# Kernel tuning notes

Hardware: AMD Instinct MI355X
Metric: run time of the kernel (lower is better)

The kernel has to match this reference:

```python
import jax, jax.numpy as jnp
import numpy as np

LEAKY_SLOPE = 0.01  # torch nn.LeakyReLU / F.leaky_relu default


def gcn_diffusion(adj, order, feat):
    # A_gcn = adj + I; sym-normalized diffusion D^-1/2 A D^-1/2 applied repeatedly
    B, N, _ = adj.shape
    A = adj + jnp.eye(N, dtype=adj.dtype)
    dinv_sqrt = jnp.sum(A, axis=2) ** -0.5  # [B, N]
    outs = []
    h = feat
    for _ in range(order):
        h = jnp.matmul(A, dinv_sqrt[..., None] * h) * dinv_sqrt[..., None]
        outs.append(h)
    return outs


def scattering_s4(adj, feat):
    # lazy random walk P = 1/2 (I + A D^-1); wavelets Psi_j = P^{2^{j-1}} - P^{2^j}
    dinv = 1.0 / jnp.sum(adj, axis=2)  # [B, N]
    p = feat
    us = []
    for _ in range(8):  # powers P^1 .. P^8
        p = 0.5 * p + 0.5 * jnp.matmul(adj, dinv[..., None] * p)
        us.append(p)
    h1 = feat - us[0]      # I - P
    h2 = us[0] - us[1]     # P - P^2
    h3 = us[1] - us[3]     # P^2 - P^4
    h4 = us[3] - us[7]     # P^4 - P^8
    return h1, h2, h3, h4


def sctconv(X, adj, W1, b1, W2, b2, a, moment):
    leaky = lambda x: jax.nn.leaky_relu(x, LEAKY_SLOPE)
    h = X  # [B, N, F]
    hA, hA2, hA3 = gcn_diffusion(adj, 3, X)
    hA, hA2, hA3 = leaky(hA), leaky(hA2), leaky(hA3)
    s1, s2, s3, s4 = scattering_s4(adj, X)
    mom = jnp.asarray(moment, dtype=X.dtype)
    s1 = jnp.abs(s1) ** mom
    s2 = jnp.abs(s2) ** mom
    s3 = jnp.abs(s3) ** mom
    s4 = jnp.abs(s4) ** mom
    # NOTE: original concatenates only (hA, hA2, s1..s4) -> 6 branches; hA3 is unused.
    h_all = jnp.stack([hA, hA2, s1, s2, s3, s4], axis=1)  # [B, 6, N, F]
    h_b = jnp.broadcast_to(h[:, None], h_all.shape)        # [B, 6, N, F]
    a_input = jnp.concatenate([h_b, h_all], axis=3)        # [B, 6, N, 2F]
    e = jnp.einsum('bknc,c->bkn', jax.nn.relu(a_input), a[:, 0])  # [B, 6, N]
    attention = jax.nn.softmax(e, axis=1)[..., None]       # [B, 6, N, 1]
    h_prime = jnp.mean(attention * h_all, axis=1)          # [B, N, F]
    out = leaky(h_prime @ W1.T + b1)
    out = leaky(out @ W2.T + b2)
    return out


def setup_inputs() -> dict:
    key = jax.random.key(0)
    kx, ka, k1, k2, k3, k4, k5 = jax.random.split(key, 7)
    B, N, F = 8, 4096, 64
    X = jax.random.normal(kx, (B, N, F), dtype=jnp.float32)
    adj = jax.random.uniform(ka, (B, N, N), dtype=jnp.float32)
    s = 1.0 / np.sqrt(F)
    W1 = jax.random.uniform(k1, (F, F), minval=-s, maxval=s, dtype=jnp.float32)
    b1 = jax.random.uniform(k2, (F,), minval=-s, maxval=s, dtype=jnp.float32)
    W2 = jax.random.uniform(k3, (F, F), minval=-s, maxval=s, dtype=jnp.float32)
    b2 = jax.random.uniform(k4, (F,), minval=-s, maxval=s, dtype=jnp.float32)
    a = jax.random.normal(k5, (2 * F, 1), dtype=jnp.float32) * 0.1
    return {"X": X, "adj": adj, "W1": W1, "b1": b1, "W2": W2, "b2": b2, "a": a, "moment": 1}


def reference(X, adj, W1, b1, W2, b2, a, moment):
    return sctconv(X, adj, W1, b1, W2, b2, a, moment)
```

## Files before the change

### kernel.cpp

```cpp
#include <hip/hip_runtime.h>
#include <hip/hip_bf16.h>
#include <cstdio>
#include <cstdint>

#define BB 8
#define NN 4096
#define FF 64

typedef __attribute__((ext_vector_type(8))) short bf16x8;
typedef __attribute__((ext_vector_type(4))) float f32x4;

__device__ __forceinline__ unsigned short f2bf(float f){
  unsigned int u = __float_as_uint(f);
  u += 0x7FFFu + ((u >> 16) & 1u);
  return (unsigned short)(u >> 16);
}

__device__ __forceinline__ float leaky01(float x){ return x > 0.f ? x : 0.01f * x; }


__global__ __launch_bounds__(256) void k_convert(const float* __restrict__ adj,
    unsigned short* __restrict__ At, float* __restrict__ dinv, float* __restrict__ dsq)
{
  const int bid = blockIdx.x;
  const int b = bid & 7, mt = bid >> 3, m0 = mt * 64;
  const int tid = threadIdx.x;
  const int r = tid >> 3, g = tid & 7;
  const float* src0 = adj + ((size_t)b * NN + m0 + r) * NN + ((g ^ (r & 7)) << 3);
  const float* src1 = src0 + (size_t)32 * NN;
  unsigned short* dst0 = At + (size_t)bid * 262144 + (((r)      * 8 + g) << 3);
  unsigned short* dst1 = At + (size_t)bid * 262144 + (((r + 32) * 8 + g) << 3);
  float s0 = 0.f, s1 = 0.f;
  for (int t = 0; t < 64; ++t){
    const float* p0 = src0 + t * 64;
    float4 a = *(const float4*)p0, c = *(const float4*)(p0 + 4);
    s0 += ((a.x + a.y) + (a.z + a.w)) + ((c.x + c.y) + (c.z + c.w));
    bf16x8 v;
    v[0]=(short)f2bf(a.x); v[1]=(short)f2bf(a.y); v[2]=(short)f2bf(a.z); v[3]=(short)f2bf(a.w);
    v[4]=(short)f2bf(c.x); v[5]=(short)f2bf(c.y); v[6]=(short)f2bf(c.z); v[7]=(short)f2bf(c.w);
    *(bf16x8*)(dst0 + (size_t)t * 4096) = v;
    const float* p1 = src1 + t * 64;
    float4 e = *(const float4*)p1, h = *(const float4*)(p1 + 4);
    s1 += ((e.x + e.y) + (e.z + e.w)) + ((h.x + h.y) + (h.z + h.w));
    bf16x8 u;
    u[0]=(short)f2bf(e.x); u[1]=(short)f2bf(e.y); u[2]=(short)f2bf(e.z); u[3]=(short)f2bf(e.w);
    u[4]=(short)f2bf(h.x); u[5]=(short)f2bf(h.y); u[6]=(short)f2bf(h.z); u[7]=(short)f2bf(h.w);
    *(bf16x8*)(dst1 + (size_t)t * 4096) = u;
  }
  s0 += __shfl_xor(s0, 1); s0 += __shfl_xor(s0, 2); s0 += __shfl_xor(s0, 4);
  s1 += __shfl_xor(s1, 1); s1 += __shfl_xor(s1, 2); s1 += __shfl_xor(s1, 4);
  if (g == 0){
    dinv[(size_t)b * NN + m0 + r] = 1.0f / s0;
    dsq [(size_t)b * NN + m0 + r] = 1.0f / sqrtf(s0 + 1.0f);
    dinv[(size_t)b * NN + m0 + 32 + r] = 1.0f / s1;
    dsq [(size_t)b * NN + m0 + 32 + r] = 1.0f / sqrtf(s1 + 1.0f);
  }
}

__global__ __launch_bounds__(256) void k_prep(const float* __restrict__ X,
    const float* __restrict__ dinv, const float* __restrict__ dsq,
    unsigned short* __restrict__ Bt)
{
  const int b = blockIdx.y, n0 = blockIdx.x * 64, tid = threadIdx.x;
  __shared__ unsigned short tg[64][68], ts[64][68];
  #pragma unroll
  for (int i = 0; i < 4; ++i){
    int idx = i * 256 + tid, n = idx >> 4, c4 = (idx & 15) * 4;
    size_t rb = (size_t)b * NN + n0 + n;
    float4 x = *(const float4*)(X + rb * 64 + c4);
    float di = dinv[b * NN + n0 + n], dv = dsq[b * NN + n0 + n];
    tg[c4 + 0][n] = f2bf(dv * x.x); tg[c4 + 1][n] = f2bf(dv * x.y);
    tg[c4 + 2][n] = f2bf(dv * x.z); tg[c4 + 3][n] = f2bf(dv * x.w);
    ts[c4 + 0][n] = f2bf(di * x.x); ts[c4 + 1][n] = f2bf(di * x.y);
    ts[c4 + 2][n] = f2bf(di * x.z); ts[c4 + 3][n] = f2bf(di * x.w);
  }
  __syncthreads();
  const int t = n0 >> 6;
  #pragma unroll
  for (int it = 0; it < 8; ++it){
    int idx = it * 256 + tid;
    int half = idx & 1, l = (idx >> 1) & 63, kk = (idx >> 7) & 1, ct = (idx >> 8) & 7;
    int cl = ((ct & 3) << 4) + (l & 15);
    int nl = kk * 32 + ((l >> 4) << 3) + half * 4;
    ushort4 v = (ct < 4) ? *(const ushort4*)&tg[cl][nl] : *(const ushort4*)&ts[cl][nl];
    *(ushort4*)(Bt + ((((size_t)b * 8 + ct) * 64 + t) * 2 + kk) * 512 + (l << 3) + half * 4) = v;
  }
}

template<int NC>
__global__ __launch_bounds__(256, 2) void k_gemm_fused(
    const unsigned short* __restrict__ At,
    const unsigned short* __restrict__ BtR, int ct0,
    const float* __restrict__ sprev, float* __restrict__ P, float* __restrict__ snap,
    const float* __restrict__ dinv, int writeVtS,
    const float* __restrict__ gprev, float* __restrict__ gout,
    const float* __restrict__ dsq, int writeVtG,
    unsigned short* __restrict__ BtW)
{
  constexpr int NF = NC / 64;
  __shared__ __align__(16) unsigned short As[4][64 * 64];
  const int bid = blockIdx.x;
  const int b = bid & 7, mt = bid >> 3, m0 = mt * 64;
  const int tid = threadIdx.x;
  const int w = tid >> 6, l = tid & 63;
  const int r0 = l & 15, hq = l >> 4, sw = r0 & 7;
  const unsigned short* Atile = At + (size_t)bid * 262144;
  const unsigned short* Bb0 = BtR + (((size_t)b * 8 + ct0 + w * NF) * 64) * 1024 + (l << 3);
  const unsigned short* Bb1 = Bb0 + (size_t)64 * 1024;

  auto stageA = [&](int buf, int t){
    const unsigned short* gp0 = Atile + (size_t)t * 4096 + (tid << 3);
    __builtin_amdgcn_global_load_lds((const __attribute__((address_space(1))) void*)gp0,
        (__attribute__((address_space(3))) void*)(&As[buf][tid << 3]), 16, 0, 0);
    __builtin_amdgcn_global_load_lds((const __attribute__((address_space(1))) void*)(gp0 + 2048),
        (__attribute__((address_space(3))) void*)(&As[buf][(256 + tid) << 3]), 16, 0, 0);
  };

  f32x4 acc[4][NF];
  #pragma unroll
  for (int mi = 0; mi < 4; ++mi)
    #pragma unroll
    for (int ni = 0; ni < NF; ++ni)
      #pragma unroll
      for (int j = 0; j < 4; ++j) acc[mi][ni][j] = 0.f;

  #define VMW(N) asm volatile("s_waitcnt vmcnt(" #N ")" ::: "memory")
  #define BARX do{ __builtin_amdgcn_s_barrier(); asm volatile("" ::: "memory"); }while(0)

  if constexpr (NC == 64){
    bf16x8 b0[2], b1[2], b2[2], b3[2];
    #define LDB1(PB, T) do{ \
      PB[0] = *(const bf16x8*)(Bb0 + (size_t)(T) * 1024); \
      PB[1] = *(const bf16x8*)(Bb0 + (size_t)(T) * 1024 + 512); }while(0)
    #define CMP64(IB, PB) do{ \
      const unsigned short* asb = &As[(IB)][0]; \
      _Pragma("unroll") for (int kk = 0; kk < 2; ++kk){ \
        const int g8 = ((kk * 4 + hq) ^ sw) << 3; \
        _Pragma("unroll") for (int mi = 0; mi < 4; ++mi){ \
          bf16x8 af = *(const bf16x8*)&asb[(mi * 16 + r0) * 64 + g8]; \
          acc[mi][0] = __builtin_amdgcn_mfma_f32_16x16x32_bf16(af, PB[kk], acc[mi][0], 0, 0, 0); \
        } } }while(0)
    #define SUB64(T, BC, BL, N) do{ \
      if ((T) + 2 < 64){ LDB1(BL, (T) + 2); stageA(((T) + 2) & 3, (T) + 2); } \
      VMW(N); BARX; CMP64((T) & 3, BC); asm volatile("" ::: "memory"); }while(0)

    stageA(0, 0); stageA(1, 1);
    LDB1(b0, 0); LDB1(b1, 1);
    SUB64(0, b0, b2, 6);
    SUB64(1, b1, b3, 8);
    #pragma unroll 1
    for (int T0 = 2; T0 <= 58; T0 += 4){
      SUB64(T0 + 0, b2, b0, 8);
      SUB64(T0 + 1, b3, b1, 8);
      SUB64(T0 + 2, b0, b2, 8);
      SUB64(T0 + 3, b1, b3, 8);
    }
    SUB64(62, b2, b0, 4);
    SUB64(63, b3, b1, 0);
  } else {
    bf16x8 b0[2][2], b1[2][2];
    #define LDB2(PB, T) do{ \
      PB[0][0] = *(const bf16x8*)(Bb0 + (size_t)(T) * 1024); \
      PB[0][1] = *(const bf16x8*)(Bb0 + (size_t)(T) * 1024 + 512); \
      PB[1][0] = *(const bf16x8*)(Bb1 + (size_t)(T) * 1024); \
      PB[1][1] = *(const bf16x8*)(Bb1 + (size_t)(T) * 1024 + 512); }while(0)
    #define CMP128(IB, PB) do{ \
      const unsigned short* asb = &As[(IB)][0]; \
      _Pragma("unroll") for (int kk = 0; kk < 2; ++kk){ \
        const int g8 = ((kk * 4 + hq) ^ sw) << 3; \
        _Pragma("unroll") for (int mi = 0; mi < 4; ++mi){ \
          bf16x8 af = *(const bf16x8*)&asb[(mi * 16 + r0) * 64 + g8]; \
          acc[mi][0] = __builtin_amdgcn_mfma_f32_16x16x32_bf16(af, PB[0][kk], acc[mi][0], 0, 0, 0); \
          acc[mi][1] = __builtin_amdgcn_mfma_f32_16x16x32_bf16(af, PB[1][kk], acc[mi][1], 0, 0, 0); \
        } } }while(0)
    #define SUB128(T, BC, BL, N) do{ \
      if ((T) + 1 < 64) LDB2(BL, (T) + 1); \
      if ((T) + 2 < 64) stageA(((T) + 2) & 3, (T) + 2); \
      VMW(N); BARX; CMP128((T) & 3, BC); asm volatile("" ::: "memory"); }while(0)

    stageA(0, 0); stageA(1, 1);
    LDB2(b0, 0);
    SUB128(0, b0, b1, 6);
    #pragma unroll 1
    for (int T0 = 1; T0 <= 59; T0 += 2){
      SUB128(T0 + 0, b1, b0, 8);
      SUB128(T0 + 1, b0, b1, 8);
    }
    SUB128(61, b1, b0, 8);
    SUB128(62, b0, b1, 6);
    SUB128(63, b1, b0, 0);
  }

  const bool isScat = (NC == 64) || (w >= 2);
  if (isScat){
    const int wS = (NC == 64) ? w : (w - 2);
    #pragma unroll
    for (int mi = 0; mi < 4; ++mi){
      const int rb = m0 + mi * 16 + hq * 4;
      const size_t rowb = (size_t)b * NN + rb;
      float4 dv4 = *(const float4*)(dinv + (size_t)b * NN + rb);
      #pragma unroll
      for (int ni = 0; ni < NF; ++ni){
        const int cs = wS * 16 * NF + ni * 16 + r0;
        float pn[4];
        #pragma unroll
        for (int j = 0; j < 4; ++j){
          float pv = sprev[(rowb + j) * 64 + cs];
          pn[j] = 0.5f * (pv + acc[mi][ni][j]);
          P[(rowb + j) * 64 + cs] = pn[j];
        }
        if (snap){
          #pragma unroll
          for (int j = 0; j < 4; ++j) snap[(rowb + j) * 64 + cs] = pn[j];
        }
        if (writeVtS){
          const int ct = 4 + wS * NF + ni;
          const int tp = rb >> 6, kkp = (rb >> 5) & 1;
          const int lp = r0 + 16 * ((rb >> 3) & 3), hf = (rb >> 2) & 1;
          ushort4 vv = make_ushort4(f2bf(dv4.x * pn[0]), f2bf(dv4.y * pn[1]),
                                    f2bf(dv4.z * pn[2]), f2bf(dv4.w * pn[3]));
          *(ushort4*)(BtW + ((((size_t)b * 8 + ct) * 64 + tp) * 2 + kkp) * 512
                          + (lp << 3) + hf * 4) = vv;
        }
      }
    }
  }
  if constexpr (NC == 128){
    if (!isScat){
      #pragma unroll
      for (int mi = 0; mi < 4; ++mi){
        const int rb = m0 + mi * 16 + hq * 4;
        const size_t rowb = (size_t)b * NN + rb;
        float4 dq4 = *(const float4*)(dsq + (size_t)b * NN + rb);
        #pragma unroll
        for (int ni = 0; ni < NF; ++ni){
          const int cg = w * 16 * NF + ni * 16 + r0;
          float hn[4];
          const float dq[4] = {dq4.x, dq4.y, dq4.z, dq4.w};
          #pragma unroll
          for (int j = 0; j < 4; ++j){
            float hv = gprev[(rowb + j) * 64 + cg];
            hn[j] = (acc[mi][ni][j] + dq[j] * hv) * dq[j];
            gout[(rowb + j) * 64 + cg] = hn[j];
          }
          if (writeVtG){
            const int ct = w * NF + ni;
            const int tp = rb >> 6, kkp = (rb >> 5) & 1;
            const int lp = r0 + 16 * ((rb >> 3) & 3), hf = (rb >> 2) & 1;
            ushort4 vv = make_ushort4(f2bf(dq[0] * hn[0]), f2bf(dq[1] * hn[1]),
                                      f2bf(dq[2] * hn[2]), f2bf(dq[3] * hn[3]));
            *(ushort4*)(BtW + ((((size_t)b * 8 + ct) * 64 + tp) * 2 + kkp) * 512
                            + (lp << 3) + hf * 4) = vv;
          }
        }
      }
    }
  }
}

__global__ __launch_bounds__(256) void k_attn(
    const float* __restrict__ X,  const float* __restrict__ hA, const float* __restrict__ hA2,
    const float* __restrict__ U1, const float* __restrict__ U2, const float* __restrict__ U4,
    const float* __restrict__ U8, const float* __restrict__ W1, const float* __restrict__ b1,
    const float* __restrict__ W2, const float* __restrict__ b2, const float* __restrict__ av,
    const int* __restrict__ momp, float* __restrict__ out)
{
  __shared__ float W1s[64][65], W2s[64][65];
  __shared__ float a1s[64], a2s[64], b1s[64], b2s[64];
  __shared__ float hp[4][64], o1[4][64];
  const int tid = threadIdx.x;
  for (int e = tid; e < 4096; e += 256){
    W1s[e >> 6][e & 63] = W1[e];
    W2s[e >> 6][e & 63] = W2[e];
  }
  if (tid < 64){ a1s[tid] = av[tid]; a2s[tid] = av[64 + tid]; b1s[tid] = b1[tid]; b2s[tid] = b2[tid]; }
  __syncthreads();
  const int w = tid >> 6, l = tid & 63;
  size_t row = (size_t)blockIdx.x * 4 + w;
  size_t off = row * 64 + l;
  float x  = X[off];
  float u1 = U1[off], u2 = U2[off], u4 = U4[off], u8 = U8[off];
  float br[6];
  br[0] = leaky01(hA[off]);
  br[1] = leaky01(hA2[off]);
  float d1 = fabsf(x - u1), d2 = fabsf(u1 - u2), d3 = fabsf(u2 - u4), d4 = fabsf(u4 - u8);
  int mom = *momp;
  if (mom == 1){ br[2] = d1; br[3] = d2; br[4] = d3; br[5] = d4; }
  else {
    float m = (float)mom;
    br[2] = powf(d1, m); br[3] = powf(d2, m); br[4] = powf(d3, m); br[5] = powf(d4, m);
  }
  float v = fmaxf(x, 0.f) * a1s[l];
  for (int o = 32; o; o >>= 1) v += __shfl_xor(v, o);
  float base = v;
  float e[6];
  #pragma unroll
  for (int k = 0; k < 6; ++k){
    float t = fmaxf(br[k], 0.f) * a2s[l];
    for (int o = 32; o; o >>= 1) t += __shfl_xor(t, o);
    e[k] = base + t;
  }
  float mx = e[0];
  #pragma unroll
  for (int k = 1; k < 6; ++k) mx = fmaxf(mx, e[k]);
  float s = 0.f, att[6];
  #pragma unroll
  for (int k = 0; k < 6; ++k){ att[k] = expf(e[k] - mx); s += att[k]; }
  float inv = 1.0f / (6.0f * s);
  float hpv = 0.f;
  #pragma unroll
  for (int k = 0; k < 6; ++k) hpv += att[k] * br[k];
  hpv *= inv;
  hp[w][l] = hpv;
  __syncthreads();
  float acc = b1s[l];
  #pragma unroll 8
  for (int c = 0; c < 64; ++c) acc += hp[w][c] * W1s[l][c];
  o1[w][l] = leaky01(acc);
  __syncthreads();
  float acc2 = b2s[l];
  #pragma unroll 8
  for (int c = 0; c < 64; ++c) acc2 += o1[w][c] * W2s[l][c];
  out[off] = leaky01(acc2);
}

static constexpr size_t OFF_ADJB = 0;
static constexpr size_t OFF_VTA  = OFF_ADJB + (size_t)BB * NN * NN * 2;
static constexpr size_t OFF_VTB  = OFF_VTA  + (size_t)BB * 128 * NN * 2;
static constexpr size_t OFF_HA   = OFF_VTB  + (size_t)BB * 128 * NN * 2;
static constexpr size_t OFF_HA2  = OFF_HA   + (size_t)BB * NN * 64 * 4;
static constexpr size_t OFF_P    = OFF_HA2  + (size_t)BB * NN * 64 * 4;
static constexpr size_t OFF_U1   = OFF_P    + (size_t)BB * NN * 64 * 4;
static constexpr size_t OFF_U2   = OFF_U1   + (size_t)BB * NN * 64 * 4;
static constexpr size_t OFF_U4   = OFF_U2   + (size_t)BB * NN * 64 * 4;
static constexpr size_t OFF_U8   = OFF_U4   + (size_t)BB * NN * 64 * 4;
static constexpr size_t OFF_DINV = OFF_U8   + (size_t)BB * NN * 64 * 4;
static constexpr size_t OFF_DS   = OFF_DINV + (size_t)BB * NN * 4;
static constexpr size_t WS_NEED  = OFF_DS   + (size_t)BB * NN * 4;

extern "C" void kernel_launch(void* const* d_in, const int* in_sizes, int n_in,
                              void* d_out, int out_size, void* d_ws, size_t ws_size,
                              hipStream_t stream)
{
  const float* X   = (const float*)d_in[0];
  const float* adj = (const float*)d_in[1];
  const float* W1  = (const float*)d_in[2];
  const float* b1  = (const float*)d_in[3];
  const float* W2  = (const float*)d_in[4];
  const float* b2  = (const float*)d_in[5];
  const float* av  = (const float*)d_in[6];
  const int*  momp = (const int*)d_in[7];
  float* out = (float*)d_out;

  if (ws_size < WS_NEED){
    fprintf(stderr, "kernel_launch: workspace too small: %zu < %zu\n", ws_size, WS_NEED);
    return;
  }
  char* w = (char*)d_ws;
  unsigned short* At  = (unsigned short*)(w + OFF_ADJB);
  unsigned short* vtA = (unsigned short*)(w + OFF_VTA);
  unsigned short* vtB = (unsigned short*)(w + OFF_VTB);
  float* hA   = (float*)(w + OFF_HA);
  float* hA2  = (float*)(w + OFF_HA2);
  float* P    = (float*)(w + OFF_P);
  float* U1   = (float*)(w + OFF_U1);
  float* U2   = (float*)(w + OFF_U2);
  float* U4   = (float*)(w + OFF_U4);
  float* U8   = (float*)(w + OFF_U8);
  float* dinv = (float*)(w + OFF_DINV);
  float* dsq  = (float*)(w + OFF_DS);

  k_convert<<<512, 256, 0, stream>>>(adj, At, dinv, dsq);
  dim3 tg64(NN / 64, BB);
  k_prep<<<tg64, 256, 0, stream>>>(X, dinv, dsq, vtA);

  k_gemm_fused<128><<<512, 256, 0, stream>>>(At, vtA, 0,
      X, P, U1, dinv, 1, X, hA, dsq, 1, vtB);
  k_gemm_fused<128><<<512, 256, 0, stream>>>(At, vtB, 0,
      P, P, U2, dinv, 1, hA, hA2, dsq, 0, vtA);
  unsigned short* vr = vtA;
  unsigned short* vw = vtB;
  for (int k = 3; k <= 8; ++k){
    float* snap = (k == 4) ? U4 : nullptr;
    float* pdst = (k == 8) ? U8 : P;
    k_gemm_fused<64><<<512, 256, 0, stream>>>(At, vr, 4,
        P, pdst, snap, dinv, (k < 8) ? 1 : 0, nullptr, nullptr, nullptr, 0, vw);
    unsigned short* t = vr; vr = vw; vw = t;
  }

  k_attn<<<BB * NN / 4, 256, 0, stream>>>(X, hA, hA2, U1, U2, U4, U8,
                                          W1, b1, W2, b2, av, momp, out);
}
```

Before: 696.7 us.

## Process two K-tiles per barrier in NC=64 GEMM with 8-deep LDS ring

For the 64-column GEMM variant, the A-tile LDS ring grows from 4 to 8 buffers and the main loop handles two K-tiles per barrier instead of one, prefetching two A tiles and two B fragments ahead. This halves the number of barriers and waitcnt stalls per block and deepens the prefetch. In exchange, LDS use doubles to 64 KB for that variant, which may reduce occupancy from two blocks per CU, and more B registers are held live.

```diff
diff --git a/kernel.cpp b/kernel.cpp
--- a/kernel.cpp
+++ b/kernel.cpp
@@ -98,7 +98,8 @@
     unsigned short* __restrict__ BtW)
 {
   constexpr int NF = NC / 64;
-  __shared__ __align__(16) unsigned short As[4][64 * 64];
+  constexpr int AD = (NC == 64) ? 8 : 4;
+  __shared__ __align__(16) unsigned short As[AD][64 * 64];
   const int bid = blockIdx.x;
   const int b = bid & 7, mt = bid >> 3, m0 = mt * 64;
   const int tid = threadIdx.x;
@@ -128,35 +129,47 @@
   #define BARX do{ __builtin_amdgcn_s_barrier(); asm volatile("" ::: "memory"); }while(0)
 
   if constexpr (NC == 64){
-    bf16x8 b0[2], b1[2], b2[2], b3[2];
-    #define LDB1(PB, T) do{ \
-      PB[0] = *(const bf16x8*)(Bb0 + (size_t)(T) * 1024); \
-      PB[1] = *(const bf16x8*)(Bb0 + (size_t)(T) * 1024 + 512); }while(0)
-    #define CMP64(IB, PB) do{ \
-      const unsigned short* asb = &As[(IB)][0]; \
-      _Pragma("unroll") for (int kk = 0; kk < 2; ++kk){ \
-        const int g8 = ((kk * 4 + hq) ^ sw) << 3; \
-        _Pragma("unroll") for (int mi = 0; mi < 4; ++mi){ \
-          bf16x8 af = *(const bf16x8*)&asb[(mi * 16 + r0) * 64 + g8]; \
-          acc[mi][0] = __builtin_amdgcn_mfma_f32_16x16x32_bf16(af, PB[kk], acc[mi][0], 0, 0, 0); \
-        } } }while(0)
-    #define SUB64(T, BC, BL, N) do{ \
-      if ((T) + 2 < 64){ LDB1(BL, (T) + 2); stageA(((T) + 2) & 3, (T) + 2); } \
-      VMW(N); BARX; CMP64((T) & 3, BC); asm volatile("" ::: "memory"); }while(0)
-
-    stageA(0, 0); stageA(1, 1);
-    LDB1(b0, 0); LDB1(b1, 1);
-    SUB64(0, b0, b2, 6);
-    SUB64(1, b1, b3, 8);
+    bf16x8 bA[4], bB[4];
+    auto LDBX = [&](bf16x8 (&PB)[4], int t2){
+      PB[0] = *(const bf16x8*)(Bb0 + (size_t)t2 * 1024);
+      PB[1] = *(const bf16x8*)(Bb0 + (size_t)t2 * 1024 + 512);
+      PB[2] = *(const bf16x8*)(Bb0 + (size_t)(t2 + 1) * 1024);
+      PB[3] = *(const bf16x8*)(Bb0 + (size_t)(t2 + 1) * 1024 + 512);
+    };
+    auto CMPT = [&](int ib, bf16x8 pb0, bf16x8 pb1){
+      const unsigned short* asb = &As[ib][0];
+      #pragma unroll
+      for (int kk = 0; kk < 2; ++kk){
+        const int g8 = ((kk * 4 + hq) ^ sw) << 3;
+        bf16x8 pb = kk ? pb1 : pb0;
+        #pragma unroll
+        for (int mi = 0; mi < 4; ++mi){
+          bf16x8 af = *(const bf16x8*)&asb[(mi * 16 + r0) * 64 + g8];
+          acc[mi][0] = __builtin_amdgcn_mfma_f32_16x16x32_bf16(af, pb, acc[mi][0], 0, 0, 0);
+        }
+      }
+    };
+    #define SS(S, BC, BN, N) do{ \
+      if (2*(S)+4 < 64){ stageA((2*(S)+4)&7, 2*(S)+4); stageA((2*(S)+5)&7, 2*(S)+5); } \
+      if (2*(S)+2 < 64){ LDBX(BN, 2*(S)+2); } \
+      VMW(N); BARX; \
+      CMPT((2*(S))&7, BC[0], BC[1]); \
+      CMPT((2*(S)+1)&7, BC[2], BC[3]); \
+      asm volatile("" ::: "memory"); \
+    }while(0)
+
+    stageA(0, 0); stageA(1, 1); stageA(2, 2); stageA(3, 3);
+    LDBX(bA, 0);
+    SS(0, bA, bB, 8);
     #pragma unroll 1
-    for (int T0 = 2; T0 <= 58; T0 += 4){
-      SUB64(T0 + 0, b2, b0, 8);
-      SUB64(T0 + 1, b3, b1, 8);
-      SUB64(T0 + 2, b0, b2, 8);
-      SUB64(T0 + 3, b1, b3, 8);
+    for (int S = 1; S < 29; S += 2){
+      SS(S,     bB, bA, 8);
+      SS(S + 1, bA, bB, 8);
     }
-    SUB64(62, b2, b0, 4);
-    SUB64(63, b3, b1, 0);
+    SS(29, bB, bA, 8);
+    SS(30, bA, bB, 4);
+    SS(31, bB, bA, 0);
+    #undef SS
   } else {
     bf16x8 b0[2][2], b1[2][2];
     #define LDB2(PB, T) do{ \
@@ -189,6 +202,9 @@
     SUB128(61, b1, b0, 8);
     SUB128(62, b0, b1, 6);
     SUB128(63, b1, b0, 0);
+    #undef SUB128
+    #undef CMP128
+    #undef LDB2
   }
 
   const bool isScat = (NC == 64) || (w >= 2);
```

Measured after the change: 691.3 us. Within noise of the previous version (-0.8%).
